# Kernel optimization log

Measured on AMD Instinct MI355X. Metric: run time of the kernel, lower is better.

## Reference

```python
import jax, jax.numpy as jnp
import numpy as np

H = 512  # hidden_dim

def setup_inputs() -> dict:
    key = jax.random.key(0)
    k1, k2, k3, k4, k5 = jax.random.split(key, 5)
    B, S = 32, 2048
    hidden = jax.random.normal(k1, (B, 2 * H), dtype=jnp.float32)
    encoder_outputs = jax.random.normal(k2, (B, S, 2 * H), dtype=jnp.float32)
    # nn.Linear(4H, H): weight [H, 4H], bias [H]
    W = jax.random.normal(k3, (H, 4 * H), dtype=jnp.float32) / np.sqrt(4 * H)
    b = jnp.zeros((H,), dtype=jnp.float32)
    v = jax.random.normal(k4, (H,), dtype=jnp.float32) / np.sqrt(H)
    return {"hidden": hidden, "encoder_outputs": encoder_outputs, "W": W, "b": b, "v": v}

def reference(hidden, encoder_outputs, W, b, v):
    B, S, _ = encoder_outputs.shape
    # concat repeated decoder hidden with encoder outputs: [B, S, 4H]
    hidden_rep = jnp.broadcast_to(hidden[:, None, :], (B, S, hidden.shape[-1]))
    cat = jnp.concatenate([hidden_rep, encoder_outputs], axis=-1)
    energy = jnp.tanh(jnp.einsum('bsf,hf->bsh', cat, W) + b)  # [B, S, H]
    scores = jnp.einsum('bsh,h->bs', energy, v)               # [B, S]
    attn = jax.nn.softmax(scores, axis=1)                     # softmax over seq
    context = jnp.einsum('bsd,bs->bd', encoder_outputs, attn) # [B, 2H]
    return context
```

## Files before the change

kernel.cpp:

```cpp
#include <hip/hip_runtime.h>


typedef __fp16   half2v __attribute__((ext_vector_type(2)));
typedef _Float16 half8  __attribute__((ext_vector_type(8)));
typedef __attribute__((ext_vector_type(4)))  float f4;
typedef __attribute__((ext_vector_type(16))) float f16v;
typedef __attribute__((ext_vector_type(4)))  unsigned int uint4v;

__device__ __forceinline__ void gload_lds16(const void* g, void* l) {
    __builtin_amdgcn_global_load_lds(
        (const __attribute__((address_space(1))) unsigned int*)g,
        (__attribute__((address_space(3))) unsigned int*)l, 16, 0, 0);
}
__device__ __forceinline__ unsigned int bc2(half2v h) {
    return __builtin_bit_cast(unsigned int, h);
}
#define MEMPIN asm volatile("" ::: "memory")

__global__ __launch_bounds__(256) void prep_kernel(
    const float* __restrict__ hidden, const float* __restrict__ W,
    const float* __restrict__ bias, float* __restrict__ u,
    unsigned short* __restrict__ w2) {
    __shared__ float hid_s[1024];
    if (blockIdx.x < 256) {
        int g = blockIdx.x * 256 + threadIdx.x;
        int kk = g >> 11, id = g & 2047;
        int ntg = id >> 7, kh = (id >> 6) & 1, l = id & 63;
        int h = (ntg << 5) + (l & 31);
        int kg = 1024 + (kk << 5) + (kh << 4) + ((l >> 5) << 3);
        const float* src = W + (size_t)h * 2048 + kg;
        f4 x0 = *(const f4*)src;
        f4 x1 = *(const f4*)(src + 4);
        half8 vh;
        #pragma unroll
        for (int j = 0; j < 4; ++j) vh[j] = (_Float16)x0[j];
        #pragma unroll
        for (int j = 0; j < 4; ++j) vh[4 + j] = (_Float16)x1[j];
        ((half8*)w2)[g] = vh;
    } else {
        const int t = threadIdx.x;
        const int blk = (int)blockIdx.x - 256;
        const int b = blk >> 3, hg = blk & 7;
        ((f4*)hid_s)[t] = ((const f4*)(hidden + ((size_t)b << 10)))[t];
        __syncthreads();
        const int w = t >> 6, lane = t & 63;
        const f4* hid4 = (const f4*)hid_s;
        #pragma unroll 2
        for (int i = 0; i < 16; ++i) {
            int h = (hg << 6) + (w << 4) + i;
            const f4* wr = (const f4*)(W + (size_t)h * 2048);
            float p = 0.f;
            #pragma unroll
            for (int i2 = 0; i2 < 4; ++i2) {
                f4 w4 = wr[lane + (i2 << 6)];
                f4 h4 = hid4[lane + (i2 << 6)];
                p += w4[0]*h4[0] + w4[1]*h4[1] + w4[2]*h4[2] + w4[3]*h4[3];
            }
            #pragma unroll
            for (int off = 1; off < 64; off <<= 1) p += __shfl_xor(p, off);
            if (lane == 0) u[((size_t)b << 9) + h] = bias[h] + p;
        }
    }
}

__global__ __launch_bounds__(256, 3) void score_kernel(
    const float* __restrict__ enc, const unsigned short* __restrict__ w2,
    const float* __restrict__ u, const float* __restrict__ v,
    float* __restrict__ scores_part) {
    __shared__ short Ahi[2048], Alo[2048];
    __shared__ short Bs[8192];
    __shared__ float u_s[256], v_s[256];
    __shared__ float partial[4][64];

    const int tid  = threadIdx.x;
    const int wl   = tid >> 6, lane = tid & 63;
    const int col  = lane & 31;
    const int sblk = blockIdx.x >> 1, hh = blockIdx.x & 1;
    const int row0 = sblk * 64;
    const int b    = row0 >> 11;
    const float* encB = enc + (size_t)row0 * 1024;

    u_s[tid] = u[(b << 9) + (hh << 8) + tid];
    v_s[tid] = v[(hh << 8) + tid];

    f16v acc[2][2];
    #pragma unroll
    for (int mt = 0; mt < 2; ++mt)
        #pragma unroll
        for (int nt = 0; nt < 2; ++nt)
            #pragma unroll
            for (int r = 0; r < 16; ++r) acc[mt][nt][r] = 0.f;

    const int s_mt = tid >> 7, s_kh = (tid >> 6) & 1, s_l = tid & 63;
    const int s_row = (s_mt << 5) + (s_l & 31);
    const int s_kb  = (s_kh << 4) + ((s_l >> 5) << 3);
    const float* aSrc = encB + (size_t)s_row * 1024 + s_kb;

    const char* bBase = (const char*)w2 + (hh << 14) + (wl << 12) + lane * 16;
    char* bdst = (char*)Bs + (wl << 12);

    const half8* Ah8 = (const half8*)Ahi;
    const half8* Al8 = (const half8*)Alo;
    const half8* Bh8 = (const half8*)Bs;

#define STAGE_B(kkex) do {                                                    \
        const char* bs_ = bBase + (size_t)(kkex) * 32768;                     \
        gload_lds16(bs_,        bdst);                                        \
        gload_lds16(bs_ + 1024, bdst + 1024);                                 \
        gload_lds16(bs_ + 2048, bdst + 2048);                                 \
        gload_lds16(bs_ + 3072, bdst + 3072);                                 \
    } while (0)

#define CVT_WRITE_A(r0, r1) do {                                              \
        half2v h01 = __builtin_amdgcn_cvt_pkrtz(r0[0], r0[1]);                \
        half2v h23 = __builtin_amdgcn_cvt_pkrtz(r0[2], r0[3]);                \
        half2v h45 = __builtin_amdgcn_cvt_pkrtz(r1[0], r1[1]);                \
        half2v h67 = __builtin_amdgcn_cvt_pkrtz(r1[2], r1[3]);                \
        half2v l01 = __builtin_amdgcn_cvt_pkrtz(r0[0] - (float)h01[0], r0[1] - (float)h01[1]); \
        half2v l23 = __builtin_amdgcn_cvt_pkrtz(r0[2] - (float)h23[0], r0[3] - (float)h23[1]); \
        half2v l45 = __builtin_amdgcn_cvt_pkrtz(r1[0] - (float)h45[0], r1[1] - (float)h45[1]); \
        half2v l67 = __builtin_amdgcn_cvt_pkrtz(r1[2] - (float)h67[0], r1[3] - (float)h67[1]); \
        uint4v hp_ = {bc2(h01), bc2(h23), bc2(h45), bc2(h67)};                \
        uint4v lp_ = {bc2(l01), bc2(l23), bc2(l45), bc2(l67)};                \
        ((uint4v*)Ahi)[tid] = hp_;                                            \
        ((uint4v*)Alo)[tid] = lp_;                                            \
    } while (0)

#define COMPUTE() do {                                                        \
        _Pragma("unroll")                                                     \
        for (int kh = 0; kh < 2; ++kh) {                                      \
            half8 ah0 = Ah8[(kh << 6) + lane];                                \
            half8 ah1 = Ah8[128 + (kh << 6) + lane];                          \
            half8 al0 = Al8[(kh << 6) + lane];                                \
            half8 al1 = Al8[128 + (kh << 6) + lane];                          \
            _Pragma("unroll")                                                 \
            for (int nt = 0; nt < 2; ++nt) {                                  \
                int ntl = (wl << 1) + nt;                                     \
                half8 b8 = Bh8[((ntl << 1) + kh) * 64 + lane];                \
                acc[0][nt] = __builtin_amdgcn_mfma_f32_32x32x16_f16(ah0, b8, acc[0][nt], 0, 0, 0); \
                acc[0][nt] = __builtin_amdgcn_mfma_f32_32x32x16_f16(al0, b8, acc[0][nt], 0, 0, 0); \
                acc[1][nt] = __builtin_amdgcn_mfma_f32_32x32x16_f16(ah1, b8, acc[1][nt], 0, 0, 0); \
                acc[1][nt] = __builtin_amdgcn_mfma_f32_32x32x16_f16(al1, b8, acc[1][nt], 0, 0, 0); \
            }                                                                 \
        }                                                                     \
    } while (0)

#define ITER(kkex, cx0, cx1, lx0, lx1) do {                                   \
        __builtin_amdgcn_s_barrier();                                         \
        STAGE_B(kkex);                                                        \
        MEMPIN;                                                               \
        int kn_ = (kkex) + 1; if (kn_ > 31) kn_ = 31;                         \
        lx0 = *(const f4*)(aSrc + (kn_ << 5));                                \
        lx1 = *(const f4*)(aSrc + (kn_ << 5) + 4);                            \
        MEMPIN;                                                               \
        CVT_WRITE_A(cx0, cx1);                                                \
        asm volatile("s_waitcnt vmcnt(2) lgkmcnt(0)" ::: "memory");           \
        __builtin_amdgcn_s_barrier();                                         \
        __builtin_amdgcn_sched_barrier(0);                                    \
        COMPUTE();                                                            \
    } while (0)

    f4 xa0 = *(const f4*)(aSrc);
    f4 xa1 = *(const f4*)(aSrc + 4);
    f4 xb0, xb1;
    asm volatile("s_waitcnt lgkmcnt(0)" ::: "memory");

    #pragma unroll 1
    for (int kk = 0; kk < 32; kk += 2) {
        ITER(kk,     xa0, xa1, xb0, xb1);
        ITER(kk + 1, xb0, xb1, xa0, xa1);
    }

#undef ITER
#undef COMPUTE
#undef CVT_WRITE_A
#undef STAGE_B

    const int rhalf = (lane >> 5) << 2;
    #pragma unroll
    for (int mt = 0; mt < 2; ++mt) {
        #pragma unroll
        for (int reg = 0; reg < 16; ++reg) {
            float ssum = 0.f;
            #pragma unroll
            for (int nt = 0; nt < 2; ++nt) {
                int hl = (((wl << 1) + nt) << 5) + col;
                float x = u_s[hl] + acc[mt][nt][reg];
                float t = __expf(2.f * x);
                float th = 1.f - 2.f / (t + 1.f);
                ssum += v_s[hl] * th;
            }
            ssum += __shfl_xor(ssum, 1);
            ssum += __shfl_xor(ssum, 2);
            ssum += __shfl_xor(ssum, 4);
            ssum += __shfl_xor(ssum, 8);
            ssum += __shfl_xor(ssum, 16);
            if (col == 0)
                partial[wl][(mt << 5) + (reg & 3) + ((reg >> 2) << 3) + rhalf] = ssum;
        }
    }
    __syncthreads();
    if (tid < 64) {
        float s = partial[0][tid] + partial[1][tid] + partial[2][tid] + partial[3][tid];
        scores_part[(hh << 16) + row0 + tid] = s;
    }
}

__global__ __launch_bounds__(256) void softmax_kernel(float* scores_part) {
    __shared__ float wredm[4], wreds[4];
    const int t = threadIdx.x, b = blockIdx.x;
    const int wid = t >> 6, lane = t & 63;
    float* s0 = scores_part + ((size_t)b << 11);
    const float* s1 = s0 + 65536;

    float vals[8];
    float mx = -1e30f;
    #pragma unroll
    for (int i = 0; i < 8; ++i) {
        int idx = t + (i << 8);
        vals[i] = s0[idx] + s1[idx];
        mx = fmaxf(mx, vals[i]);
    }
    #pragma unroll
    for (int off = 1; off < 64; off <<= 1) mx = fmaxf(mx, __shfl_xor(mx, off));
    if (lane == 0) wredm[wid] = mx;
    __syncthreads();
    mx = fmaxf(fmaxf(wredm[0], wredm[1]), fmaxf(wredm[2], wredm[3]));

    float e[8], lsum = 0.f;
    #pragma unroll
    for (int i = 0; i < 8; ++i) {
        e[i] = __expf(vals[i] - mx);
        lsum += e[i];
    }
    #pragma unroll
    for (int off = 1; off < 64; off <<= 1) lsum += __shfl_xor(lsum, off);
    if (lane == 0) wreds[wid] = lsum;
    __syncthreads();
    const float inv = 1.f / (wreds[0] + wreds[1] + wreds[2] + wreds[3]);
    #pragma unroll
    for (int i = 0; i < 8; ++i) s0[t + (i << 8)] = e[i] * inv;
}

__global__ __launch_bounds__(256) void ctx_partial_kernel(
    const float* __restrict__ enc, const float* __restrict__ attn,
    float* __restrict__ partials) {
    __shared__ float a_s[64];
    const int t = threadIdx.x;
    const int b = blockIdx.x >> 5, sc = blockIdx.x & 31;
    if (t < 64) a_s[t] = attn[((size_t)b << 11) + (sc << 6) + t];
    __syncthreads();

    f4 a0 = (f4){0.f, 0.f, 0.f, 0.f};
    f4 a1 = (f4){0.f, 0.f, 0.f, 0.f};
    f4 a2 = (f4){0.f, 0.f, 0.f, 0.f};
    f4 a3 = (f4){0.f, 0.f, 0.f, 0.f};
    const f4* erow = ((const f4*)(enc + ((size_t)b * 2048 + (sc << 6)) * 1024)) + t;
    #pragma unroll 4
    for (int i = 0; i < 64; i += 4) {
        a0 += a_s[i]     * erow[(size_t)i << 8];
        a1 += a_s[i + 1] * erow[((size_t)(i + 1)) << 8];
        a2 += a_s[i + 2] * erow[((size_t)(i + 2)) << 8];
        a3 += a_s[i + 3] * erow[((size_t)(i + 3)) << 8];
    }
    f4 a = (a0 + a1) + (a2 + a3);
    f4* dst = (f4*)(partials + (((size_t)(sc << 5) + b) << 10));
    dst[t] = a;
}

__global__ __launch_bounds__(256) void ctx_reduce_kernel(
    const float* __restrict__ partials, float* __restrict__ out) {
    int i = blockIdx.x * 256 + threadIdx.x;
    float s = 0.f;
    #pragma unroll
    for (int sc = 0; sc < 32; ++sc) s += partials[sc * 32768 + i];
    out[i] = s;
}

extern "C" void kernel_launch(void* const* d_in, const int* in_sizes, int n_in,
                              void* d_out, int out_size, void* d_ws, size_t ws_size,
                              hipStream_t stream) {
    const float* hidden = (const float*)d_in[0];
    const float* enc    = (const float*)d_in[1];
    const float* W      = (const float*)d_in[2];
    const float* bias   = (const float*)d_in[3];
    const float* v      = (const float*)d_in[4];
    float* out = (float*)d_out;
    char* ws = (char*)d_ws;

    float* u            = (float*)(ws);
    float* scores_part  = (float*)(ws + 65536);
    float* partials     = (float*)(ws + 589824);
    unsigned short* w2  = (unsigned short*)(ws + 4784128);

    prep_kernel<<<512, 256, 0, stream>>>(hidden, W, bias, u, w2);
    score_kernel<<<2048, 256, 0, stream>>>(enc, w2, u, v, scores_part);
    softmax_kernel<<<32, 256, 0, stream>>>(scores_part);
    ctx_partial_kernel<<<1024, 256, 0, stream>>>(enc, scores_part, partials);
    ctx_reduce_kernel<<<128, 256, 0, stream>>>(partials, out);
}
```

Before: 520.2 us.

## Double-buffer LDS tiles to overlap staging with MFMA compute, remap block order

Doubles the LDS A/B buffers so the next k-step's B tile (async global→LDS) and converted A tile are written into the alternate buffer while MFMAs consume the current one. This drops one barrier per iteration and hides load latency behind compute. It also permutes the block index so consecutive workgroups spread across XCDs/batches, which changes L2 locality for W and enc. In exchange, LDS use per block roughly doubles, which may reduce occupancy below the 3 blocks/CU target.

```diff
diff --git a/kernel.cpp b/kernel.cpp
--- a/kernel.cpp
+++ b/kernel.cpp
@@ -67,15 +67,17 @@
     const float* __restrict__ enc, const unsigned short* __restrict__ w2,
     const float* __restrict__ u, const float* __restrict__ v,
     float* __restrict__ scores_part) {
-    __shared__ short Ahi[2048], Alo[2048];
-    __shared__ short Bs[8192];
+    __shared__ short Ahi[2][2048], Alo[2][2048];
+    __shared__ short Bs[2][8192];
     __shared__ float u_s[256], v_s[256];
     __shared__ float partial[4][64];
 
     const int tid  = threadIdx.x;
     const int wl   = tid >> 6, lane = tid & 63;
     const int col  = lane & 31;
-    const int sblk = blockIdx.x >> 1, hh = blockIdx.x & 1;
+    const int bid  = blockIdx.x;
+    const int lid  = ((bid & 7) << 8) + (bid >> 3);
+    const int sblk = lid >> 1, hh = lid & 1;
     const int row0 = sblk * 64;
     const int b    = row0 >> 11;
     const float* encB = enc + (size_t)row0 * 1024;
@@ -97,21 +99,17 @@
     const float* aSrc = encB + (size_t)s_row * 1024 + s_kb;
 
     const char* bBase = (const char*)w2 + (hh << 14) + (wl << 12) + lane * 16;
-    char* bdst = (char*)Bs + (wl << 12);
-
-    const half8* Ah8 = (const half8*)Ahi;
-    const half8* Al8 = (const half8*)Alo;
-    const half8* Bh8 = (const half8*)Bs;
-
-#define STAGE_B(kkex) do {                                                    \
+
+#define STAGE_B(buf, kkex) do {                                               \
         const char* bs_ = bBase + (size_t)(kkex) * 32768;                     \
-        gload_lds16(bs_,        bdst);                                        \
-        gload_lds16(bs_ + 1024, bdst + 1024);                                 \
-        gload_lds16(bs_ + 2048, bdst + 2048);                                 \
-        gload_lds16(bs_ + 3072, bdst + 3072);                                 \
+        char* bd_ = (char*)(&Bs[buf][0]) + (wl << 12);                        \
+        gload_lds16(bs_,        bd_);                                         \
+        gload_lds16(bs_ + 1024, bd_ + 1024);                                  \
+        gload_lds16(bs_ + 2048, bd_ + 2048);                                  \
+        gload_lds16(bs_ + 3072, bd_ + 3072);                                  \
     } while (0)
 
-#define CVT_WRITE_A(r0, r1) do {                                              \
+#define CVT_WRITE_A(buf, r0, r1) do {                                         \
         half2v h01 = __builtin_amdgcn_cvt_pkrtz(r0[0], r0[1]);                \
         half2v h23 = __builtin_amdgcn_cvt_pkrtz(r0[2], r0[3]);                \
         half2v h45 = __builtin_amdgcn_cvt_pkrtz(r1[0], r1[1]);                \
@@ -122,21 +120,24 @@
         half2v l67 = __builtin_amdgcn_cvt_pkrtz(r1[2] - (float)h67[0], r1[3] - (float)h67[1]); \
         uint4v hp_ = {bc2(h01), bc2(h23), bc2(h45), bc2(h67)};                \
         uint4v lp_ = {bc2(l01), bc2(l23), bc2(l45), bc2(l67)};                \
-        ((uint4v*)Ahi)[tid] = hp_;                                            \
-        ((uint4v*)Alo)[tid] = lp_;                                            \
+        ((uint4v*)(&Ahi[buf][0]))[tid] = hp_;                                 \
+        ((uint4v*)(&Alo[buf][0]))[tid] = lp_;                                 \
     } while (0)
 
-#define COMPUTE() do {                                                        \
+#define COMPUTE(buf) do {                                                     \
+        const half8* Ah8_ = (const half8*)(&Ahi[buf][0]);                     \
+        const half8* Al8_ = (const half8*)(&Alo[buf][0]);                     \
+        const half8* Bh8_ = (const half8*)(&Bs[buf][0]);                      \
         _Pragma("unroll")                                                     \
         for (int kh = 0; kh < 2; ++kh) {                                      \
-            half8 ah0 = Ah8[(kh << 6) + lane];                                \
-            half8 ah1 = Ah8[128 + (kh << 6) + lane];                          \
-            half8 al0 = Al8[(kh << 6) + lane];                                \
-            half8 al1 = Al8[128 + (kh << 6) + lane];                          \
+            half8 ah0 = Ah8_[(kh << 6) + lane];                               \
+            half8 ah1 = Ah8_[128 + (kh << 6) + lane];                         \
+            half8 al0 = Al8_[(kh << 6) + lane];                               \
+            half8 al1 = Al8_[128 + (kh << 6) + lane];                         \
             _Pragma("unroll")                                                 \
             for (int nt = 0; nt < 2; ++nt) {                                  \
                 int ntl = (wl << 1) + nt;                                     \
-                half8 b8 = Bh8[((ntl << 1) + kh) * 64 + lane];                \
+                half8 b8 = Bh8_[((ntl << 1) + kh) * 64 + lane];               \
                 acc[0][nt] = __builtin_amdgcn_mfma_f32_32x32x16_f16(ah0, b8, acc[0][nt], 0, 0, 0); \
                 acc[0][nt] = __builtin_amdgcn_mfma_f32_32x32x16_f16(al0, b8, acc[0][nt], 0, 0, 0); \
                 acc[1][nt] = __builtin_amdgcn_mfma_f32_32x32x16_f16(ah1, b8, acc[1][nt], 0, 0, 0); \
@@ -145,30 +146,38 @@
         }                                                                     \
     } while (0)
 
-#define ITER(kkex, cx0, cx1, lx0, lx1) do {                                   \
-        __builtin_amdgcn_s_barrier();                                         \
-        STAGE_B(kkex);                                                        \
+#define ITER(kkex, buf, cx0, cx1, lx0, lx1) do {                              \
+        int kb_ = (kkex) + 1; if (kb_ > 31) kb_ = 31;                         \
+        STAGE_B((buf) ^ 1, kb_);                                              \
         MEMPIN;                                                               \
-        int kn_ = (kkex) + 1; if (kn_ > 31) kn_ = 31;                         \
+        int kn_ = (kkex) + 2; if (kn_ > 31) kn_ = 31;                         \
         lx0 = *(const f4*)(aSrc + (kn_ << 5));                                \
         lx1 = *(const f4*)(aSrc + (kn_ << 5) + 4);                            \
         MEMPIN;                                                               \
-        CVT_WRITE_A(cx0, cx1);                                                \
+        CVT_WRITE_A((buf) ^ 1, cx0, cx1);                                     \
+        COMPUTE(buf);                                                         \
         asm volatile("s_waitcnt vmcnt(2) lgkmcnt(0)" ::: "memory");           \
         __builtin_amdgcn_s_barrier();                                         \
         __builtin_amdgcn_sched_barrier(0);                                    \
-        COMPUTE();                                                            \
     } while (0)
 
     f4 xa0 = *(const f4*)(aSrc);
     f4 xa1 = *(const f4*)(aSrc + 4);
-    f4 xb0, xb1;
-    asm volatile("s_waitcnt lgkmcnt(0)" ::: "memory");
+    MEMPIN;
+    STAGE_B(0, 0);
+    MEMPIN;
+    f4 xb0 = *(const f4*)(aSrc + 32);
+    f4 xb1 = *(const f4*)(aSrc + 36);
+    MEMPIN;
+    CVT_WRITE_A(0, xa0, xa1);
+    asm volatile("s_waitcnt vmcnt(2) lgkmcnt(0)" ::: "memory");
+    __builtin_amdgcn_s_barrier();
+    __builtin_amdgcn_sched_barrier(0);
 
     #pragma unroll 1
     for (int kk = 0; kk < 32; kk += 2) {
-        ITER(kk,     xa0, xa1, xb0, xb1);
-        ITER(kk + 1, xb0, xb1, xa0, xa1);
+        ITER(kk,     0, xb0, xb1, xa0, xa1);
+        ITER(kk + 1, 1, xa0, xa1, xb0, xb1);
     }
 
 #undef ITER
```

After: 535.5 us. +2.9%, slower.
